# Optimization experiments

Hardware: AMD Instinct MI355X
Metric: run time of the kernel (lower is better)

## Reference

```python
import jax, jax.numpy as jnp
import numpy as np

NUM_NODES = 100000
NUM_EDGES = 1600000
IN_DIM = 128
OUT_DIM = 128


def setup_inputs() -> dict:
    key = jax.random.key(0)
    k_x, k_e, k_wn, k_bn, k_ws, k_bs = jax.random.split(key, 6)
    x = jax.random.normal(k_x, (NUM_NODES, IN_DIM), dtype=jnp.float32)
    edge_index = jax.random.randint(k_e, (2, NUM_EDGES), 0, NUM_NODES, dtype=jnp.int64)
    s = 1.0 / np.sqrt(IN_DIM)
    W_neigh = jax.random.uniform(k_wn, (OUT_DIM, IN_DIM), dtype=jnp.float32, minval=-s, maxval=s)
    b_neigh = jax.random.uniform(k_bn, (OUT_DIM,), dtype=jnp.float32, minval=-s, maxval=s)
    W_self = jax.random.uniform(k_ws, (OUT_DIM, IN_DIM), dtype=jnp.float32, minval=-s, maxval=s)
    b_self = jax.random.uniform(k_bs, (OUT_DIM,), dtype=jnp.float32, minval=-s, maxval=s)
    return {"x": x, "edge_index": edge_index, "W_neigh": W_neigh, "b_neigh": b_neigh,
            "W_self": W_self, "b_self": b_self}


def reference(x, edge_index, W_neigh, b_neigh, W_self, b_self):
    src, dst = edge_index[0], edge_index[1]
    # gather source node feats per edge, sum-aggregate per destination node
    msgs = x[src]  # [E, d]
    neigh = jax.ops.segment_sum(msgs, dst, num_segments=x.shape[0])  # [N, d]
    neigh_proj = neigh @ W_neigh.T + b_neigh  # [N, out]
    self_proj = x @ W_self.T + b_self         # [N, out]
    return neigh_proj + self_proj
```

## Files before the change

kernel.cpp:

```cpp
#include <hip/hip_runtime.h>
#include <hip/hip_bf16.h>

#define NN 100000
#define NE 1600000
#define DIM 128
#define BM 64
#define CAP 28
#define OVFCAP 131072
#define CVT_BLK 1024
#define SC_BLK 1024

typedef __attribute__((ext_vector_type(8))) short short8;
typedef __attribute__((ext_vector_type(4))) float f32x4;
typedef __attribute__((ext_vector_type(4))) unsigned short ushort4v;

__device__ __forceinline__ unsigned short f2bf(float f) {
  union { float f; unsigned u; } v; v.f = f;
  unsigned r = v.u + 0x7fffu + ((v.u >> 16) & 1u);
  return (unsigned short)(r >> 16);
}
__device__ __forceinline__ float bf2f(unsigned short h) {
  union { unsigned u; float f; } v; v.u = ((unsigned)h) << 16;
  return v.f;
}

__global__ __launch_bounds__(256) void prep_scatter_kernel(
    const float* __restrict__ x, const int* __restrict__ ei,
    const float* __restrict__ Wn, const float* __restrict__ bn,
    const float* __restrict__ Ws, const float* __restrict__ bs,
    unsigned short* __restrict__ xb, unsigned short* __restrict__ wnb,
    unsigned short* __restrict__ wsb, float* __restrict__ bsum,
    int* __restrict__ cnt, int* __restrict__ ovfcnt, int2* __restrict__ ovf,
    int* __restrict__ slots) {
  int b = blockIdx.x;
  if (b < CVT_BLK) {
    int tid = b * 256 + threadIdx.x;
    const int stride = CVT_BLK * 256;
    const int NC = NN * DIM / 4;
    for (int i = tid; i < NC; i += stride) {
      f32x4 v = reinterpret_cast<const f32x4*>(x)[i];
      ushort4v u;
      u[0] = f2bf(v[0]); u[1] = f2bf(v[1]); u[2] = f2bf(v[2]); u[3] = f2bf(v[3]);
      reinterpret_cast<ushort4v*>(xb)[i] = u;
    }
    if (tid < DIM * DIM) { wnb[tid] = f2bf(Wn[tid]); wsb[tid] = f2bf(Ws[tid]); }
    if (tid < DIM) bsum[tid] = bn[tid] + bs[tid];
  } else {
    int tid = (b - CVT_BLK) * 256 + threadIdx.x;
    const int T = SC_BLK * 256;
    int ss[8], dd[8];
    bool vv[8];
    #pragma unroll
    for (int k = 0; k < 8; ++k) {
      int ee = tid + k * T;
      bool v = ee < NE;
      int s = v ? ei[ee] : 0;
      int d = v ? ei[NE + ee] : 0;
      v = v && ((unsigned)s < NN) && ((unsigned)d < NN);
      ss[k] = s; dd[k] = d; vv[k] = v;
    }
    int rr[8];
    #pragma unroll
    for (int k = 0; k < 8; ++k)
      rr[k] = vv[k] ? atomicAdd(&cnt[dd[k]], 1) : 0;
    #pragma unroll
    for (int k = 0; k < 8; ++k) {
      if (vv[k]) {
        if (rr[k] < CAP) {
          slots[dd[k] * CAP + rr[k]] = ss[k];
        } else {
          int o = atomicAdd(ovfcnt, 1);
          if (o < OVFCAP) ovf[o] = make_int2(dd[k], ss[k]);
        }
      }
    }
  }
}

__global__ __launch_bounds__(512) void fusedgemm_kernel(
    const unsigned short* __restrict__ xb,
    const int* __restrict__ cnt, const int* __restrict__ slots,
    const int2* __restrict__ ovf, const int* __restrict__ ovfcnt,
    const unsigned short* __restrict__ wnb, const unsigned short* __restrict__ wsb,
    const float* __restrict__ bsum, float* __restrict__ out) {
  __shared__ unsigned short sW[DIM * DIM];
  __shared__ unsigned short sA[BM * DIM];
  __shared__ unsigned short sX[BM * DIM];
  __shared__ int2 lovf[256];
  __shared__ int lovfn;
  const int tid = threadIdx.x;
  const int row0 = blockIdx.x * BM;

  if (tid == 0) lovfn = 0;
  #pragma unroll
  for (int it = 0; it < 2; ++it) {
    int id = it * 512 + tid;
    int r = id >> 4, c = id & 15;
    int gr = row0 + r;
    short8 v = (short8)0;
    if (gr < NN) v = *reinterpret_cast<const short8*>(xb + (size_t)gr * DIM + c * 8);
    int off = (r * 256 + c * 16) ^ ((r & 7) << 4);
    *reinterpret_cast<short8*>(reinterpret_cast<char*>(sX) + off) = v;
  }
  #pragma unroll
  for (int it = 0; it < 4; ++it) {
    int id = it * 512 + tid;
    int r = id >> 4, c = id & 15;
    short8 w = *reinterpret_cast<const short8*>(wnb + r * DIM + c * 8);
    int off = (r * 256 + c * 16) ^ ((r & 7) << 4);
    *reinterpret_cast<short8*>(reinterpret_cast<char*>(sW) + off) = w;
  }
  __syncthreads();

  {
    int ovfn = min(*ovfcnt, OVFCAP);
    for (int k = tid; k < ovfn; k += 512) {
      int2 p = ovf[k];
      if ((unsigned)(p.x - row0) < (unsigned)BM) {
        int t = atomicAdd(&lovfn, 1);
        if (t < 256) lovf[t] = p;
      }
    }
  }
  __syncthreads();

  {
    const int lg = tid >> 5, ln = tid & 31;
    int g = row0 + lg;
    int m = 0, idx = 0;
    if (g < NN) {
      m = min(cnt[g], CAP);
      if (ln < m) idx = slots[g * CAP + ln];
    }
    const int lcnt = min(lovfn, 256);
    for (int it = 0; it < 4; ++it) {
      int r = it * 16 + lg;
      int gcur = row0 + r;
      int mn = 0, idxn = 0;
      if (it < 3) {
        int gn = row0 + (it + 1) * 16 + lg;
        if (gn < NN) {
          mn = min(cnt[gn], CAP);
          if (ln < mn) idxn = slots[gn * CAP + ln];
        }
      }
      f32x4 a0 = (f32x4){0.f,0.f,0.f,0.f}, a1 = a0, a2 = a0, a3 = a0;
      f32x4 a4 = a0, a5 = a0, a6 = a0, a7 = a0;
      int e = 0;
      for (; e + 7 < m; e += 8) {
        int s0 = __shfl(idx, e, 32),     s1 = __shfl(idx, e + 1, 32);
        int s2 = __shfl(idx, e + 2, 32), s3 = __shfl(idx, e + 3, 32);
        int s4 = __shfl(idx, e + 4, 32), s5 = __shfl(idx, e + 5, 32);
        int s6 = __shfl(idx, e + 6, 32), s7 = __shfl(idx, e + 7, 32);
        ushort4v u0 = *reinterpret_cast<const ushort4v*>(xb + (size_t)s0 * DIM + ln * 4);
        ushort4v u1 = *reinterpret_cast<const ushort4v*>(xb + (size_t)s1 * DIM + ln * 4);
        ushort4v u2 = *reinterpret_cast<const ushort4v*>(xb + (size_t)s2 * DIM + ln * 4);
        ushort4v u3 = *reinterpret_cast<const ushort4v*>(xb + (size_t)s3 * DIM + ln * 4);
        ushort4v u4 = *reinterpret_cast<const ushort4v*>(xb + (size_t)s4 * DIM + ln * 4);
        ushort4v u5 = *reinterpret_cast<const ushort4v*>(xb + (size_t)s5 * DIM + ln * 4);
        ushort4v u6 = *reinterpret_cast<const ushort4v*>(xb + (size_t)s6 * DIM + ln * 4);
        ushort4v u7 = *reinterpret_cast<const ushort4v*>(xb + (size_t)s7 * DIM + ln * 4);
        #pragma unroll
        for (int j = 0; j < 4; ++j) {
          a0[j] += bf2f(u0[j]); a1[j] += bf2f(u1[j]);
          a2[j] += bf2f(u2[j]); a3[j] += bf2f(u3[j]);
          a4[j] += bf2f(u4[j]); a5[j] += bf2f(u5[j]);
          a6[j] += bf2f(u6[j]); a7[j] += bf2f(u7[j]);
        }
      }
      for (; e + 3 < m; e += 4) {
        int s0 = __shfl(idx, e, 32),     s1 = __shfl(idx, e + 1, 32);
        int s2 = __shfl(idx, e + 2, 32), s3 = __shfl(idx, e + 3, 32);
        ushort4v u0 = *reinterpret_cast<const ushort4v*>(xb + (size_t)s0 * DIM + ln * 4);
        ushort4v u1 = *reinterpret_cast<const ushort4v*>(xb + (size_t)s1 * DIM + ln * 4);
        ushort4v u2 = *reinterpret_cast<const ushort4v*>(xb + (size_t)s2 * DIM + ln * 4);
        ushort4v u3 = *reinterpret_cast<const ushort4v*>(xb + (size_t)s3 * DIM + ln * 4);
        #pragma unroll
        for (int j = 0; j < 4; ++j) {
          a0[j] += bf2f(u0[j]); a1[j] += bf2f(u1[j]);
          a2[j] += bf2f(u2[j]); a3[j] += bf2f(u3[j]);
        }
      }
      for (; e < m; ++e) {
        int s0 = __shfl(idx, e, 32);
        ushort4v u0 = *reinterpret_cast<const ushort4v*>(xb + (size_t)s0 * DIM + ln * 4);
        #pragma unroll
        for (int j = 0; j < 4; ++j) a0[j] += bf2f(u0[j]);
      }
      for (int k2 = 0; k2 < lcnt; ++k2) {
        int2 p = lovf[k2];
        if (p.x == gcur) {
          ushort4v u0 = *reinterpret_cast<const ushort4v*>(xb + (size_t)p.y * DIM + ln * 4);
          #pragma unroll
          for (int j = 0; j < 4; ++j) a0[j] += bf2f(u0[j]);
        }
      }
      a0 += a1; a2 += a3; a4 += a5; a6 += a7;
      a0 += a2; a4 += a6; a0 += a4;
      ushort4v o;
      o[0] = f2bf(a0[0]); o[1] = f2bf(a0[1]); o[2] = f2bf(a0[2]); o[3] = f2bf(a0[3]);
      int off = (r * 256 + ln * 8) ^ ((r & 7) << 4);
      *reinterpret_cast<ushort4v*>(reinterpret_cast<char*>(sA) + off) = o;
      idx = idxn; m = mn;
    }
  }
  __syncthreads();

  const int wave = tid >> 6;
  const int lane = tid & 63;
  const int wm = wave & 3, wn = wave >> 2;
  const int arow = wm * 16 + (lane & 15);
  const int kl = (lane >> 4) * 8;
  f32x4 acc[4];
  #pragma unroll
  for (int t = 0; t < 4; ++t) acc[t] = (f32x4){0.f, 0.f, 0.f, 0.f};

  #pragma unroll
  for (int ks = 0; ks < 4; ++ks) {
    int k = ks * 32 + kl;
    short8 a = *reinterpret_cast<const short8*>(
        reinterpret_cast<const char*>(sA) + ((arow * 256 + k * 2) ^ ((arow & 7) << 4)));
    #pragma unroll
    for (int t = 0; t < 4; ++t) {
      int o = (wn * 4 + t) * 16 + (lane & 15);
      short8 bfr = *reinterpret_cast<const short8*>(
          reinterpret_cast<const char*>(sW) + ((o * 256 + k * 2) ^ ((o & 7) << 4)));
      acc[t] = __builtin_amdgcn_mfma_f32_16x16x32_bf16(a, bfr, acc[t], 0, 0, 0);
    }
  }
  __syncthreads();
  #pragma unroll
  for (int it = 0; it < 4; ++it) {
    int id = it * 512 + tid;
    int r = id >> 4, c = id & 15;
    short8 w = *reinterpret_cast<const short8*>(wsb + r * DIM + c * 8);
    int off = (r * 256 + c * 16) ^ ((r & 7) << 4);
    *reinterpret_cast<short8*>(reinterpret_cast<char*>(sW) + off) = w;
  }
  __syncthreads();
  #pragma unroll
  for (int ks = 0; ks < 4; ++ks) {
    int k = ks * 32 + kl;
    short8 a = *reinterpret_cast<const short8*>(
        reinterpret_cast<const char*>(sX) + ((arow * 256 + k * 2) ^ ((arow & 7) << 4)));
    #pragma unroll
    for (int t = 0; t < 4; ++t) {
      int o = (wn * 4 + t) * 16 + (lane & 15);
      short8 bfr = *reinterpret_cast<const short8*>(
          reinterpret_cast<const char*>(sW) + ((o * 256 + k * 2) ^ ((o & 7) << 4)));
      acc[t] = __builtin_amdgcn_mfma_f32_16x16x32_bf16(a, bfr, acc[t], 0, 0, 0);
    }
  }

  #pragma unroll
  for (int t = 0; t < 4; ++t) {
    int col = (wn * 4 + t) * 16 + (lane & 15);
    float bv = bsum[col];
    #pragma unroll
    for (int reg = 0; reg < 4; ++reg) {
      int gr = row0 + wm * 16 + (lane >> 4) * 4 + reg;
      if (gr < NN) out[(size_t)gr * DIM + col] = acc[t][reg] + bv;
    }
  }
}

extern "C" void kernel_launch(void* const* d_in, const int* in_sizes, int n_in,
                              void* d_out, int out_size, void* d_ws, size_t ws_size,
                              hipStream_t stream) {
  const float* x  = (const float*)d_in[0];
  const int*   ei = (const int*)d_in[1];
  const float* Wn = (const float*)d_in[2];
  const float* bn = (const float*)d_in[3];
  const float* Ws = (const float*)d_in[4];
  const float* bs = (const float*)d_in[5];
  float* out = (float*)d_out;
  char* ws = (char*)d_ws;

  unsigned short* wnb = (unsigned short*)(ws + 0);
  unsigned short* wsb = (unsigned short*)(ws + 32768);
  float* bsum        = (float*)(ws + 65536);
  int* cnt           = (int*)(ws + 66560);
  int* ovfcnt        = (int*)(ws + 466560);
  int2* ovf          = (int2*)(ws + 466688);
  int* slots         = (int*)(ws + 1515264);
  unsigned short* xb = (unsigned short*)(ws + 12715264);

  hipMemsetAsync(cnt, 0, 400064, stream);
  prep_scatter_kernel<<<CVT_BLK + SC_BLK, 256, 0, stream>>>(
      x, ei, Wn, bn, Ws, bs, xb, wnb, wsb, bsum, cnt, ovfcnt, ovf, slots);
  fusedgemm_kernel<<<(NN + BM - 1) / BM, 512, 0, stream>>>(
      xb, cnt, slots, ovf, ovfcnt, wnb, wsb, bsum, out);
}
```

Baseline: 191.9 us.

## Pad degree counters, use nontemporal loads/stores, read self rows directly from global

Spreads the per-node degree counters four ints apart so concurrent atomics on neighbouring nodes fall in different cache lines, and enlarges the memset to match. The fp32-to-bf16 conversion and the edge-index reads now use nontemporal loads and stores. The GEMM kernel drops its shared-memory staging of self-node rows and loads the A fragments straight from global memory, which frees LDS but adds uncoalesced global reads inside the MFMA loop. The overflow buffer capacity is reduced, so inputs with many high-degree nodes could overflow it.

Result: slower. 203.0 us (+5.8%).

```diff
diff --git a/kernel.cpp b/kernel.cpp
--- a/kernel.cpp
+++ b/kernel.cpp
@@ -6,9 +6,10 @@
 #define DIM 128
 #define BM 64
 #define CAP 28
-#define OVFCAP 131072
+#define OVFCAP 16384
 #define CVT_BLK 1024
 #define SC_BLK 1024
+#define CSTRIDE 4
 
 typedef __attribute__((ext_vector_type(8))) short short8;
 typedef __attribute__((ext_vector_type(4))) float f32x4;
@@ -38,10 +39,10 @@
     const int stride = CVT_BLK * 256;
     const int NC = NN * DIM / 4;
     for (int i = tid; i < NC; i += stride) {
-      f32x4 v = reinterpret_cast<const f32x4*>(x)[i];
+      f32x4 v = __builtin_nontemporal_load(reinterpret_cast<const f32x4*>(x) + i);
       ushort4v u;
       u[0] = f2bf(v[0]); u[1] = f2bf(v[1]); u[2] = f2bf(v[2]); u[3] = f2bf(v[3]);
-      reinterpret_cast<ushort4v*>(xb)[i] = u;
+      __builtin_nontemporal_store(u, reinterpret_cast<ushort4v*>(xb) + i);
     }
     if (tid < DIM * DIM) { wnb[tid] = f2bf(Wn[tid]); wsb[tid] = f2bf(Ws[tid]); }
     if (tid < DIM) bsum[tid] = bn[tid] + bs[tid];
@@ -54,15 +55,15 @@
     for (int k = 0; k < 8; ++k) {
       int ee = tid + k * T;
       bool v = ee < NE;
-      int s = v ? ei[ee] : 0;
-      int d = v ? ei[NE + ee] : 0;
+      int s = v ? __builtin_nontemporal_load(ei + ee) : 0;
+      int d = v ? __builtin_nontemporal_load(ei + NE + ee) : 0;
       v = v && ((unsigned)s < NN) && ((unsigned)d < NN);
       ss[k] = s; dd[k] = d; vv[k] = v;
     }
     int rr[8];
     #pragma unroll
     for (int k = 0; k < 8; ++k)
-      rr[k] = vv[k] ? atomicAdd(&cnt[dd[k]], 1) : 0;
+      rr[k] = vv[k] ? atomicAdd(&cnt[dd[k] * CSTRIDE], 1) : 0;
     #pragma unroll
     for (int k = 0; k < 8; ++k) {
       if (vv[k]) {
@@ -85,23 +86,12 @@
     const float* __restrict__ bsum, float* __restrict__ out) {
   __shared__ unsigned short sW[DIM * DIM];
   __shared__ unsigned short sA[BM * DIM];
-  __shared__ unsigned short sX[BM * DIM];
   __shared__ int2 lovf[256];
   __shared__ int lovfn;
   const int tid = threadIdx.x;
   const int row0 = blockIdx.x * BM;
 
   if (tid == 0) lovfn = 0;
-  #pragma unroll
-  for (int it = 0; it < 2; ++it) {
-    int id = it * 512 + tid;
-    int r = id >> 4, c = id & 15;
-    int gr = row0 + r;
-    short8 v = (short8)0;
-    if (gr < NN) v = *reinterpret_cast<const short8*>(xb + (size_t)gr * DIM + c * 8);
-    int off = (r * 256 + c * 16) ^ ((r & 7) << 4);
-    *reinterpret_cast<short8*>(reinterpret_cast<char*>(sX) + off) = v;
-  }
   #pragma unroll
   for (int it = 0; it < 4; ++it) {
     int id = it * 512 + tid;
@@ -129,7 +119,7 @@
     int g = row0 + lg;
     int m = 0, idx = 0;
     if (g < NN) {
-      m = min(cnt[g], CAP);
+      m = min(cnt[g * CSTRIDE], CAP);
       if (ln < m) idx = slots[g * CAP + ln];
     }
     const int lcnt = min(lovfn, 256);
@@ -140,7 +130,7 @@
       if (it < 3) {
         int gn = row0 + (it + 1) * 16 + lg;
         if (gn < NN) {
-          mn = min(cnt[gn], CAP);
+          mn = min(cnt[gn * CSTRIDE], CAP);
           if (ln < mn) idxn = slots[gn * CAP + ln];
         }
       }
@@ -238,17 +228,21 @@
     *reinterpret_cast<short8*>(reinterpret_cast<char*>(sW) + off) = w;
   }
   __syncthreads();
-  #pragma unroll
-  for (int ks = 0; ks < 4; ++ks) {
-    int k = ks * 32 + kl;
-    short8 a = *reinterpret_cast<const short8*>(
-        reinterpret_cast<const char*>(sX) + ((arow * 256 + k * 2) ^ ((arow & 7) << 4)));
-    #pragma unroll
-    for (int t = 0; t < 4; ++t) {
-      int o = (wn * 4 + t) * 16 + (lane & 15);
-      short8 bfr = *reinterpret_cast<const short8*>(
-          reinterpret_cast<const char*>(sW) + ((o * 256 + k * 2) ^ ((o & 7) << 4)));
-      acc[t] = __builtin_amdgcn_mfma_f32_16x16x32_bf16(a, bfr, acc[t], 0, 0, 0);
+  {
+    const int gr2 = row0 + arow;
+    const bool av = gr2 < NN;
+    #pragma unroll
+    for (int ks = 0; ks < 4; ++ks) {
+      int k = ks * 32 + kl;
+      short8 a = (short8)0;
+      if (av) a = *reinterpret_cast<const short8*>(xb + (size_t)gr2 * DIM + k);
+      #pragma unroll
+      for (int t = 0; t < 4; ++t) {
+        int o = (wn * 4 + t) * 16 + (lane & 15);
+        short8 bfr = *reinterpret_cast<const short8*>(
+            reinterpret_cast<const char*>(sW) + ((o * 256 + k * 2) ^ ((o & 7) << 4)));
+        acc[t] = __builtin_amdgcn_mfma_f32_16x16x32_bf16(a, bfr, acc[t], 0, 0, 0);
+      }
     }
   }
 
@@ -280,12 +274,12 @@
   unsigned short* wsb = (unsigned short*)(ws + 32768);
   float* bsum        = (float*)(ws + 65536);
   int* cnt           = (int*)(ws + 66560);
-  int* ovfcnt        = (int*)(ws + 466560);
-  int2* ovf          = (int2*)(ws + 466688);
-  int* slots         = (int*)(ws + 1515264);
-  unsigned short* xb = (unsigned short*)(ws + 12715264);
-
-  hipMemsetAsync(cnt, 0, 400064, stream);
+  int* ovfcnt        = (int*)(ws + 1666560);
+  int2* ovf          = (int2*)(ws + 1666624);
+  int* slots         = (int*)(ws + 1797696);
+  unsigned short* xb = (unsigned short*)(ws + 12997696);
+
+  hipMemsetAsync(cnt, 0, 1600064, stream);
   prep_scatter_kernel<<<CVT_BLK + SC_BLK, 256, 0, stream>>>(
       x, ei, Wn, bn, Ws, bs, xb, wnb, wsb, bsum, cnt, ovfcnt, ovf, slots);
   fusedgemm_kernel<<<(NN + BM - 1) / BM, 512, 0, stream>>>(
```
